# Kernel optimization log

Measured on AMD Instinct MI355X. Metric: run time of the kernel, lower is better.

## Reference

```python
import jax, jax.numpy as jnp
import numpy as np

N_NODES = 100000

def sage_conv(x, src, dst, Wl, bl, Wr):
    # PyG SAGEConv (mean aggr): out = lin_l(mean_{j in N(i)} x_j) + lin_r(x_i)
    msg = x[src]                                            # [E, d] gather
    agg = jax.ops.segment_sum(msg, dst, num_segments=N_NODES)
    cnt = jax.ops.segment_sum(jnp.ones((src.shape[0],), dtype=x.dtype), dst,
                              num_segments=N_NODES)
    agg = agg / jnp.maximum(cnt, 1.0)[:, None]              # mean over neighbors
    return agg @ Wl.T + bl + x @ Wr.T


def setup_inputs() -> dict:
    key = jax.random.key(0)
    ks = jax.random.split(key, 8)
    E = 1600000
    in_c, hid, out_c = 256, 128, 40
    x = jax.random.normal(ks[0], (N_NODES, in_c), dtype=jnp.float32)
    edge_index = jax.random.randint(ks[1], (2, E), 0, N_NODES, dtype=jnp.int64)
    s = 1.0 / np.sqrt(in_c)
    s2 = 1.0 / np.sqrt(hid)
    Wl1 = jax.random.uniform(ks[2], (hid, in_c), jnp.float32, -s, s)
    bl1 = jnp.zeros((hid,), jnp.float32)
    Wr1 = jax.random.uniform(ks[3], (hid, in_c), jnp.float32, -s, s)
    Wl2 = jax.random.uniform(ks[4], (out_c, hid), jnp.float32, -s2, s2)
    bl2 = jnp.zeros((out_c,), jnp.float32)
    Wr2 = jax.random.uniform(ks[5], (out_c, hid), jnp.float32, -s2, s2)
    return {"x": x, "edge_index": edge_index, "Wl1": Wl1, "bl1": bl1,
            "Wr1": Wr1, "Wl2": Wl2, "bl2": bl2, "Wr2": Wr2}


def reference(x, edge_index, Wl1, bl1, Wr1, Wl2, bl2, Wr2):
    src, dst = edge_index[0], edge_index[1]
    h = sage_conv(x, src, dst, Wl1, bl1, Wr1)
    h = jax.nn.relu(h)  # dropout is identity in eval mode
    h = sage_conv(h, src, dst, Wl2, bl2, Wr2)
    return jax.nn.log_softmax(h, axis=-1)
```

## Files before the change

kernel.cpp:

```cpp
#include <hip/hip_runtime.h>
#include <hip/hip_bf16.h>

#define N_NODES 100000
#define IN_C 256
#define HID 128
#define OUT_C 40

#define NPB 9
#define NPP (1 << NPB)
#define NPART ((N_NODES + NPP - 1) >> NPB)
#define CAP 16384

typedef short bf16x8 __attribute__((ext_vector_type(8)));
typedef float f32x4 __attribute__((ext_vector_type(4)));
typedef float f32x2 __attribute__((ext_vector_type(2)));

static __device__ __forceinline__ float bf2f(unsigned short u) {
    return __uint_as_float(((unsigned)u) << 16);
}
static __device__ __forceinline__ unsigned short f2bf(float f) {
    unsigned u = __float_as_uint(f);
    u += 0x7fffu + ((u >> 16) & 1u);
    return (unsigned short)(u >> 16);
}

__global__ __launch_bounds__(256) void cvtw_k(
    const float* __restrict__ Wl1, const float* __restrict__ Wr1,
    const float* __restrict__ Wl2, const float* __restrict__ Wr2,
    unsigned short* __restrict__ W1f, unsigned short* __restrict__ W2f)
{
    int gid = blockIdx.x * 256 + threadIdx.x;
    if (gid < 8192) {
        int g = gid;
        int ln = g & 63, blk = g >> 6;
        int c16 = blk >> 3, ks = blk & 7;
        int col = c16 * 16 + (ln & 15);
        int k0 = ks * 32 + (ln >> 4) * 8;
        const float* src = (col < 128) ? &Wl1[(size_t)col * 256 + k0]
                                       : &Wr1[(size_t)(col - 128) * 256 + k0];
        float4 v0 = *(const float4*)src;
        float4 v1 = *(const float4*)(src + 4);
        bf16x8 a;
        a[0] = (short)f2bf(v0.x); a[1] = (short)f2bf(v0.y);
        a[2] = (short)f2bf(v0.z); a[3] = (short)f2bf(v0.w);
        a[4] = (short)f2bf(v1.x); a[5] = (short)f2bf(v1.y);
        a[6] = (short)f2bf(v1.z); a[7] = (short)f2bf(v1.w);
        *(bf16x8*)&W1f[(size_t)g * 8] = a;
    } else if (gid < 9472) {
        int g = gid - 8192;
        int ln = g & 63, blk = g >> 6;
        int c16 = blk >> 2, ks = blk & 3;
        int col = c16 * 16 + (ln & 15);
        int k0 = ks * 32 + (ln >> 4) * 8;
        const float* src = (col < 40) ? &Wl2[(size_t)col * 128 + k0]
                                      : &Wr2[(size_t)(col - 40) * 128 + k0];
        float4 v0 = *(const float4*)src;
        float4 v1 = *(const float4*)(src + 4);
        bf16x8 a;
        a[0] = (short)f2bf(v0.x); a[1] = (short)f2bf(v0.y);
        a[2] = (short)f2bf(v0.z); a[3] = (short)f2bf(v0.w);
        a[4] = (short)f2bf(v1.x); a[5] = (short)f2bf(v1.y);
        a[6] = (short)f2bf(v1.z); a[7] = (short)f2bf(v1.w);
        *(bf16x8*)&W2f[(size_t)g * 8] = a;
    }
}

__global__ __launch_bounds__(256) void mega1_k(
    const int* __restrict__ ei, int E, int nblkS,
    int* __restrict__ pcnt, unsigned* __restrict__ pairs,
    const float* __restrict__ X,
    const unsigned short* __restrict__ Wf,
    const float* __restrict__ bias,
    unsigned* __restrict__ Yq,
    unsigned short* __restrict__ Zb,
    int M)
{
    constexpr int KP = 264;
    __shared__ unsigned short As[32][KP];
    const int bid = blockIdx.x;
    const int tx = threadIdx.x;

    if (bid < nblkS) {
        int* lh = (int*)&As[0][0];
        int* lb = lh + NPART;
        if (tx < NPART) lh[tx] = 0;
        __syncthreads();
        int base = bid * 4096;
        int n = min(4096, E - base);
        for (int i = tx; i < n; i += 256)
            atomicAdd(&lh[((unsigned)ei[E + base + i]) >> NPB], 1);
        __syncthreads();
        if (tx < NPART) {
            int c = lh[tx];
            lb[tx] = c ? atomicAdd(&pcnt[tx], c) : 0;
            lh[tx] = 0;
        }
        __syncthreads();
        for (int i = tx; i < n; i += 256) {
            unsigned src = (unsigned)ei[base + i];
            unsigned dst = (unsigned)ei[E + base + i];
            int p = dst >> NPB;
            int r = atomicAdd(&lh[p], 1);
            pairs[(size_t)p * CAP + lb[p] + r] = (src << NPB) | (dst & (NPP - 1));
        }
        return;
    }

    const int rowTile = (bid - nblkS) * 32;
    const int wc = tx >> 6, ln = tx & 63;
    const int lc = ln & 15, lk = (ln >> 4) * 8;

    float4 va[4], vb[4];
    #pragma unroll
    for (int i = 0; i < 4; ++i) {
        int g = i * 256 + tx;
        int r = g >> 5, kk = (g & 31) * 8;
        int gr = rowTile + r;
        if (gr < M) {
            const float* p = &X[(size_t)gr * 256 + kk];
            va[i] = *(const float4*)p;
            vb[i] = *(const float4*)(p + 4);
        } else {
            va[i] = make_float4(0.f, 0.f, 0.f, 0.f);
            vb[i] = make_float4(0.f, 0.f, 0.f, 0.f);
        }
    }
    #pragma unroll
    for (int i = 0; i < 4; ++i) {
        int g = i * 256 + tx;
        int r = g >> 5, kk = (g & 31) * 8;
        bf16x8 a;
        a[0] = (short)f2bf(va[i].x); a[1] = (short)f2bf(va[i].y);
        a[2] = (short)f2bf(va[i].z); a[3] = (short)f2bf(va[i].w);
        a[4] = (short)f2bf(vb[i].x); a[5] = (short)f2bf(vb[i].y);
        a[6] = (short)f2bf(vb[i].z); a[7] = (short)f2bf(vb[i].w);
        *(bf16x8*)&As[r][kk] = a;
    }
    __syncthreads();

    f32x4 acc[2][4] = {};
    #pragma unroll
    for (int ks = 0; ks < 8; ++ks) {
        int koff = ks * 32 + lk;
        bf16x8 bfr[4], af[2];
        #pragma unroll
        for (int n = 0; n < 4; ++n)
            bfr[n] = *(const bf16x8*)&Wf[(size_t)(((wc * 4 + n) * 8 + ks) * 512 + ln * 8)];
        #pragma unroll
        for (int m = 0; m < 2; ++m)
            af[m] = *(const bf16x8*)&As[m * 16 + lc][koff];
        #pragma unroll
        for (int m = 0; m < 2; ++m)
            #pragma unroll
            for (int n = 0; n < 4; ++n)
                acc[m][n] = __builtin_amdgcn_mfma_f32_16x16x32_bf16(af[m], bfr[n], acc[m][n], 0, 0, 0);
    }

    __syncthreads();
    const int lr4 = (ln >> 4) * 4;
    #pragma unroll
    for (int m = 0; m < 2; ++m) {
        int r0 = m * 16 + lr4;
        #pragma unroll
        for (int n = 0; n < 4; ++n) {
            int col = wc * 64 + n * 16 + lc;
            float b = (col >= 128) ? bias[col - 128] : 0.f;
            #pragma unroll
            for (int j = 0; j < 4; ++j)
                As[r0 + j][col] = f2bf(acc[m][n][j] + b);
        }
    }
    __syncthreads();
    #pragma unroll
    for (int i = 0; i < 4; ++i) {
        int g = i * 256 + tx;
        int r = g >> 5, c8 = (g & 31) * 8;
        int gr = rowTile + r;
        if (gr >= M) continue;
        bf16x8 v = *(const bf16x8*)&As[r][c8];
        if (c8 < 128) {
            float f0 = bf2f((unsigned short)v[0]), f1 = bf2f((unsigned short)v[1]);
            float f2 = bf2f((unsigned short)v[2]), f3 = bf2f((unsigned short)v[3]);
            float f4 = bf2f((unsigned short)v[4]), f5 = bf2f((unsigned short)v[5]);
            float f6 = bf2f((unsigned short)v[6]), f7 = bf2f((unsigned short)v[7]);
            unsigned lo = __builtin_amdgcn_cvt_pk_fp8_f32(f0, f1, 0, false);
            lo = __builtin_amdgcn_cvt_pk_fp8_f32(f2, f3, lo, true);
            unsigned hi = __builtin_amdgcn_cvt_pk_fp8_f32(f4, f5, 0, false);
            hi = __builtin_amdgcn_cvt_pk_fp8_f32(f6, f7, hi, true);
            uint2 o; o.x = lo; o.y = hi;
            *(uint2*)&Yq[(size_t)gr * 32 + (c8 >> 2)] = o;
        } else {
            *(bf16x8*)&Zb[(size_t)gr * 128 + (c8 - 128)] = v;
        }
    }
}

__global__ __launch_bounds__(256) void pbuild_k(const unsigned* __restrict__ pairs, const int* __restrict__ pcnt,
                                                unsigned* __restrict__ row_info, float* __restrict__ inv,
                                                int* __restrict__ csr, int N) {
    __shared__ int cnt[NPP];
    __shared__ int cur[NPP];
    __shared__ int wsum[4];
    int p = blockIdx.x;
    int ec = pcnt[p];
    size_t base = (size_t)p * CAP;
    int node0 = p << NPB;
    int tid = threadIdx.x;
    cnt[2 * tid] = 0; cnt[2 * tid + 1] = 0;
    __syncthreads();
    for (int e = tid; e < ec; e += 256)
        atomicAdd(&cnt[pairs[base + e] & (NPP - 1)], 1);
    __syncthreads();
    int c0 = cnt[2 * tid], c1 = cnt[2 * tid + 1];
    int s = c0 + c1;
    int lane = tid & 63, w = tid >> 6;
    int ps = s;
    #pragma unroll
    for (int off = 1; off < 64; off <<= 1) { int x = __shfl_up(ps, off); if (lane >= off) ps += x; }
    if (lane == 63) wsum[w] = ps;
    __syncthreads();
    int woff = 0;
    for (int i = 0; i < w; ++i) woff += wsum[i];
    int excl = woff + ps - s;
    int node = node0 + 2 * tid;
    int abeg = (int)base + excl;
    if (node < N) {
        row_info[node] = ((unsigned)abeg << 10) | (unsigned)min(c0, 1023);
        inv[node] = 1.f / fmaxf((float)c0, 1.f);
    }
    if (node + 1 < N) {
        row_info[node + 1] = ((unsigned)(abeg + c0) << 10) | (unsigned)min(c1, 1023);
        inv[node + 1] = 1.f / fmaxf((float)c1, 1.f);
    }
    cur[2 * tid] = excl; cur[2 * tid + 1] = excl + c0;
    __syncthreads();
    for (int e = tid; e < ec; e += 256) {
        unsigned pr = pairs[base + e];
        int r = atomicAdd(&cur[pr & (NPP - 1)], 1);
        csr[base + r] = (int)(pr >> NPB);
    }
}

__global__ __launch_bounds__(256) void gather1_k(const unsigned* __restrict__ row_info, const int* __restrict__ csr,
                                                 const unsigned* __restrict__ Yq,
                                                 unsigned short* __restrict__ Zb,
                                                 const float* __restrict__ inv, int n) {
    int node = blockIdx.x * 16 + (threadIdx.x >> 4);
    if (node >= n) return;
    int t = threadIdx.x & 15;
    unsigned info = row_info[node];
    int beg = (int)(info >> 10), end = beg + (int)(info & 1023);
    float a0 = 0.f, a1 = 0.f, a2 = 0.f, a3 = 0.f;
    float a4 = 0.f, a5 = 0.f, a6 = 0.f, a7 = 0.f;
    int e = beg;
    for (; e + 2 <= end; e += 2) {
        int s0 = csr[e], s1 = csr[e + 1];
        uint2 u0 = *(const uint2*)&Yq[(size_t)s0 * 32 + t * 2];
        uint2 u1 = *(const uint2*)&Yq[(size_t)s1 * 32 + t * 2];
        f32x2 p;
        p = __builtin_amdgcn_cvt_pk_f32_fp8(u0.x, false); a0 += p[0]; a1 += p[1];
        p = __builtin_amdgcn_cvt_pk_f32_fp8(u0.x, true);  a2 += p[0]; a3 += p[1];
        p = __builtin_amdgcn_cvt_pk_f32_fp8(u0.y, false); a4 += p[0]; a5 += p[1];
        p = __builtin_amdgcn_cvt_pk_f32_fp8(u0.y, true);  a6 += p[0]; a7 += p[1];
        p = __builtin_amdgcn_cvt_pk_f32_fp8(u1.x, false); a0 += p[0]; a1 += p[1];
        p = __builtin_amdgcn_cvt_pk_f32_fp8(u1.x, true);  a2 += p[0]; a3 += p[1];
        p = __builtin_amdgcn_cvt_pk_f32_fp8(u1.y, false); a4 += p[0]; a5 += p[1];
        p = __builtin_amdgcn_cvt_pk_f32_fp8(u1.y, true);  a6 += p[0]; a7 += p[1];
    }
    if (e < end) {
        uint2 u0 = *(const uint2*)&Yq[(size_t)csr[e] * 32 + t * 2];
        f32x2 p;
        p = __builtin_amdgcn_cvt_pk_f32_fp8(u0.x, false); a0 += p[0]; a1 += p[1];
        p = __builtin_amdgcn_cvt_pk_f32_fp8(u0.x, true);  a2 += p[0]; a3 += p[1];
        p = __builtin_amdgcn_cvt_pk_f32_fp8(u0.y, false); a4 += p[0]; a5 += p[1];
        p = __builtin_amdgcn_cvt_pk_f32_fp8(u0.y, true);  a6 += p[0]; a7 += p[1];
    }
    float iv = inv[node];
    bf16x8 z = *(const bf16x8*)&Zb[(size_t)node * HID + t * 8];
    bf16x8 h;
    h[0] = (short)f2bf(fmaxf(a0 * iv + bf2f((unsigned short)z[0]), 0.f));
    h[1] = (short)f2bf(fmaxf(a1 * iv + bf2f((unsigned short)z[1]), 0.f));
    h[2] = (short)f2bf(fmaxf(a2 * iv + bf2f((unsigned short)z[2]), 0.f));
    h[3] = (short)f2bf(fmaxf(a3 * iv + bf2f((unsigned short)z[3]), 0.f));
    h[4] = (short)f2bf(fmaxf(a4 * iv + bf2f((unsigned short)z[4]), 0.f));
    h[5] = (short)f2bf(fmaxf(a5 * iv + bf2f((unsigned short)z[5]), 0.f));
    h[6] = (short)f2bf(fmaxf(a6 * iv + bf2f((unsigned short)z[6]), 0.f));
    h[7] = (short)f2bf(fmaxf(a7 * iv + bf2f((unsigned short)z[7]), 0.f));
    *(bf16x8*)&Zb[(size_t)node * HID + t * 8] = h;
}

__global__ __launch_bounds__(256) void gemm2_k(
    const unsigned short* __restrict__ Hb,
    const unsigned short* __restrict__ Wf,
    const float* __restrict__ bias,
    unsigned* __restrict__ Y2q,
    unsigned short* __restrict__ Z2b,
    int M)
{
    constexpr int KP = 136;
    __shared__ unsigned short As[128][KP];
    const int tx = threadIdx.x;
    const int rowTile = blockIdx.x * 128;
    const int wv = tx >> 6, ln = tx & 63;
    const int lc = ln & 15, lk = (ln >> 4) * 8;

    #pragma unroll
    for (int i = 0; i < 8; ++i) {
        int g = i * 256 + tx;
        int r = g >> 4, kk = (g & 15) * 8;
        int gr = rowTile + r;
        bf16x8 a = {};
        if (gr < M) a = *(const bf16x8*)&Hb[(size_t)gr * 128 + kk];
        *(bf16x8*)&As[r][kk] = a;
    }
    __syncthreads();

    f32x4 acc[2][5] = {};
    #pragma unroll
    for (int ks = 0; ks < 4; ++ks) {
        int koff = ks * 32 + lk;
        bf16x8 bfr[5], af[2];
        #pragma unroll
        for (int n = 0; n < 5; ++n)
            bfr[n] = *(const bf16x8*)&Wf[(size_t)((n * 4 + ks) * 512 + ln * 8)];
        #pragma unroll
        for (int m = 0; m < 2; ++m)
            af[m] = *(const bf16x8*)&As[wv * 32 + m * 16 + lc][koff];
        #pragma unroll
        for (int m = 0; m < 2; ++m)
            #pragma unroll
            for (int n = 0; n < 5; ++n)
                acc[m][n] = __builtin_amdgcn_mfma_f32_16x16x32_bf16(af[m], bfr[n], acc[m][n], 0, 0, 0);
    }

    __syncthreads();
    unsigned short (*OutL)[96] = (unsigned short (*)[96])&As[0][0];
    const int lr4 = (ln >> 4) * 4;
    #pragma unroll
    for (int m = 0; m < 2; ++m) {
        int r0 = wv * 32 + m * 16 + lr4;
        #pragma unroll
        for (int n = 0; n < 5; ++n) {
            int col = n * 16 + lc;
            float b = (col >= 40) ? bias[col - 40] : 0.f;
            #pragma unroll
            for (int j = 0; j < 4; ++j)
                OutL[r0 + j][col] = f2bf(acc[m][n][j] + b);
        }
    }
    __syncthreads();
    #pragma unroll
    for (int i = 0; i < 5; ++i) {
        int g = i * 256 + tx;
        int r = g / 10, cg = g % 10;
        int c8 = cg * 8;
        int gr = rowTile + r;
        if (gr >= M) continue;
        bf16x8 v = *(const bf16x8*)&OutL[r][c8];
        if (c8 < 40) {
            float f0 = bf2f((unsigned short)v[0]), f1 = bf2f((unsigned short)v[1]);
            float f2 = bf2f((unsigned short)v[2]), f3 = bf2f((unsigned short)v[3]);
            float f4 = bf2f((unsigned short)v[4]), f5 = bf2f((unsigned short)v[5]);
            float f6 = bf2f((unsigned short)v[6]), f7 = bf2f((unsigned short)v[7]);
            unsigned lo = __builtin_amdgcn_cvt_pk_fp8_f32(f0, f1, 0, false);
            lo = __builtin_amdgcn_cvt_pk_fp8_f32(f2, f3, lo, true);
            unsigned hi = __builtin_amdgcn_cvt_pk_fp8_f32(f4, f5, 0, false);
            hi = __builtin_amdgcn_cvt_pk_fp8_f32(f6, f7, hi, true);
            uint2 o; o.x = lo; o.y = hi;
            *(uint2*)&Y2q[(size_t)gr * 10 + (c8 >> 2)] = o;
        } else {
            *(bf16x8*)&Z2b[(size_t)gr * 40 + (c8 - 40)] = v;
        }
    }
}

__global__ __launch_bounds__(256) void gather2_logsm_k(const unsigned* __restrict__ row_info, const int* __restrict__ csr,
                                                       const unsigned* __restrict__ Y2q,
                                                       const unsigned short* __restrict__ Zb,
                                                       const float* __restrict__ inv,
                                                       float* __restrict__ out, int n) {
    int node = blockIdx.x * 16 + (threadIdx.x >> 4);
    if (node >= n) return;
    int t = threadIdx.x & 15;
    float4 v = make_float4(-INFINITY, -INFINITY, -INFINITY, -INFINITY);
    if (t < 10) {
        unsigned info = row_info[node];
        int beg = (int)(info >> 10), end = beg + (int)(info & 1023);
        float a0 = 0.f, a1 = 0.f, a2 = 0.f, a3 = 0.f;
        for (int e = beg; e < end; ++e) {
            unsigned u = Y2q[(size_t)csr[e] * 10 + t];
            f32x2 p;
            p = __builtin_amdgcn_cvt_pk_f32_fp8(u, false); a0 += p[0]; a1 += p[1];
            p = __builtin_amdgcn_cvt_pk_f32_fp8(u, true);  a2 += p[0]; a3 += p[1];
        }
        float iv = inv[node];
        ushort4 z = *(const ushort4*)&Zb[(size_t)node * OUT_C + t * 4];
        v.x = a0 * iv + bf2f(z.x); v.y = a1 * iv + bf2f(z.y);
        v.z = a2 * iv + bf2f(z.z); v.w = a3 * iv + bf2f(z.w);
    }
    float m = fmaxf(fmaxf(v.x, v.y), fmaxf(v.z, v.w));
    #pragma unroll
    for (int off = 8; off; off >>= 1) m = fmaxf(m, __shfl_xor(m, off, 16));
    float s4 = 0.f;
    if (t < 10) s4 = expf(v.x - m) + expf(v.y - m) + expf(v.z - m) + expf(v.w - m);
    #pragma unroll
    for (int off = 8; off; off >>= 1) s4 += __shfl_xor(s4, off, 16);
    float ls = m + logf(s4);
    if (t < 10) {
        float4 o;
        o.x = v.x - ls; o.y = v.y - ls; o.z = v.z - ls; o.w = v.w - ls;
        *(float4*)&out[(size_t)node * OUT_C + t * 4] = o;
    }
}

extern "C" void kernel_launch(void* const* d_in, const int* in_sizes, int n_in,
                              void* d_out, int out_size, void* d_ws, size_t ws_size,
                              hipStream_t stream) {
    const float* x   = (const float*)d_in[0];
    const int*   ei  = (const int*)d_in[1];
    const float* Wl1 = (const float*)d_in[2];
    const float* bl1 = (const float*)d_in[3];
    const float* Wr1 = (const float*)d_in[4];
    const float* Wl2 = (const float*)d_in[5];
    const float* bl2 = (const float*)d_in[6];
    const float* Wr2 = (const float*)d_in[7];
    float* out = (float*)d_out;
    const int N = N_NODES;
    const int E = in_sizes[1] / 2;

    char* ws = (char*)d_ws;
    int*      pcnt     = (int*)(ws + 0x0000);
    unsigned* row_info = (unsigned*)(ws + 0x10000);
    float*    inv      = (float*)(ws + 0x80000);
    int*      csr      = (int*)(ws + 0x100000);
    unsigned* pairs    = (unsigned*)(ws + 0xE00000);
    unsigned short* Z2b = (unsigned short*)(ws + 0xE00000);
    unsigned short* W1f = (unsigned short*)(ws + 0x1B00000);
    unsigned short* W2f = (unsigned short*)(ws + 0x1B60000);
    unsigned* Yq1   = (unsigned*)(ws + 0x1C00000);
    unsigned short* Z1b = (unsigned short*)(ws + 0x3500000);
    unsigned* Y2q   = (unsigned*)(ws + 0x5200000);

    hipMemsetAsync(pcnt, 0, NPART * 4, stream);

    cvtw_k<<<37, 256, 0, stream>>>(Wl1, Wr1, Wl2, Wr2, W1f, W2f);

    int nblkS = (E + 4095) / 4096;
    int nblkG = (N + 31) / 32;
    mega1_k<<<nblkS + nblkG, 256, 0, stream>>>(ei, E, nblkS, pcnt, pairs,
                                               x, W1f, bl1, Yq1, Z1b, N);

    pbuild_k<<<NPART, 256, 0, stream>>>(pairs, pcnt, row_info, inv, csr, N);

    gather1_k<<<(N + 15) / 16, 256, 0, stream>>>(row_info, csr, Yq1, Z1b, inv, N);

    gemm2_k<<<(N + 127) / 128, 256, 0, stream>>>(Z1b, W2f, bl2, Y2q, Z2b, N);

    gather2_logsm_k<<<(N + 15) / 16, 256, 0, stream>>>(row_info, csr, Y2q, Z2b, inv, out, N);
}
```

Before: 184.9 us.

## Reorder mega1 block roles, raise MFMA priority, widen pbuild to 512 threads

Three separate tweaks. The fused mega1 kernel now runs its GEMM row-tile blocks first and the edge-scatter blocks after them, which changes how work is scheduled across CUs. s_setprio brackets the MFMA loops in both GEMM kernels so those waves get issue priority. pbuild uses 512 threads with one node per thread instead of 256 threads handling two nodes each, which shortens the serial per-thread work and widens the scan and atomic loops, at some cost in occupancy and launch shape.

```diff
diff --git a/kernel.cpp b/kernel.cpp
--- a/kernel.cpp
+++ b/kernel.cpp
@@ -66,7 +66,7 @@
 }
 
 __global__ __launch_bounds__(256) void mega1_k(
-    const int* __restrict__ ei, int E, int nblkS,
+    const int* __restrict__ ei, int E, int nblkG,
     int* __restrict__ pcnt, unsigned* __restrict__ pairs,
     const float* __restrict__ X,
     const unsigned short* __restrict__ Wf,
@@ -80,12 +80,12 @@
     const int bid = blockIdx.x;
     const int tx = threadIdx.x;
 
-    if (bid < nblkS) {
+    if (bid >= nblkG) {
         int* lh = (int*)&As[0][0];
         int* lb = lh + NPART;
         if (tx < NPART) lh[tx] = 0;
         __syncthreads();
-        int base = bid * 4096;
+        int base = (bid - nblkG) * 4096;
         int n = min(4096, E - base);
         for (int i = tx; i < n; i += 256)
             atomicAdd(&lh[((unsigned)ei[E + base + i]) >> NPB], 1);
@@ -106,7 +106,7 @@
         return;
     }
 
-    const int rowTile = (bid - nblkS) * 32;
+    const int rowTile = bid * 32;
     const int wc = tx >> 6, ln = tx & 63;
     const int lc = ln & 15, lk = (ln >> 4) * 8;
 
@@ -149,11 +149,13 @@
         #pragma unroll
         for (int m = 0; m < 2; ++m)
             af[m] = *(const bf16x8*)&As[m * 16 + lc][koff];
+        __builtin_amdgcn_s_setprio(1);
         #pragma unroll
         for (int m = 0; m < 2; ++m)
             #pragma unroll
             for (int n = 0; n < 4; ++n)
                 acc[m][n] = __builtin_amdgcn_mfma_f32_16x16x32_bf16(af[m], bfr[n], acc[m][n], 0, 0, 0);
+        __builtin_amdgcn_s_setprio(0);
     }
 
     __syncthreads();
@@ -195,46 +197,41 @@
     }
 }
 
-__global__ __launch_bounds__(256) void pbuild_k(const unsigned* __restrict__ pairs, const int* __restrict__ pcnt,
+__global__ __launch_bounds__(512) void pbuild_k(const unsigned* __restrict__ pairs, const int* __restrict__ pcnt,
                                                 unsigned* __restrict__ row_info, float* __restrict__ inv,
                                                 int* __restrict__ csr, int N) {
     __shared__ int cnt[NPP];
     __shared__ int cur[NPP];
-    __shared__ int wsum[4];
+    __shared__ int wsum[8];
     int p = blockIdx.x;
     int ec = pcnt[p];
     size_t base = (size_t)p * CAP;
     int node0 = p << NPB;
     int tid = threadIdx.x;
-    cnt[2 * tid] = 0; cnt[2 * tid + 1] = 0;
-    __syncthreads();
-    for (int e = tid; e < ec; e += 256)
+    cnt[tid] = 0;
+    __syncthreads();
+    for (int e = tid; e < ec; e += 512)
         atomicAdd(&cnt[pairs[base + e] & (NPP - 1)], 1);
     __syncthreads();
-    int c0 = cnt[2 * tid], c1 = cnt[2 * tid + 1];
-    int s = c0 + c1;
+    int c0 = cnt[tid];
     int lane = tid & 63, w = tid >> 6;
-    int ps = s;
+    int ps = c0;
     #pragma unroll
     for (int off = 1; off < 64; off <<= 1) { int x = __shfl_up(ps, off); if (lane >= off) ps += x; }
     if (lane == 63) wsum[w] = ps;
     __syncthreads();
     int woff = 0;
     for (int i = 0; i < w; ++i) woff += wsum[i];
-    int excl = woff + ps - s;
-    int node = node0 + 2 * tid;
+    int excl = woff + ps - c0;
+    int node = node0 + tid;
     int abeg = (int)base + excl;
     if (node < N) {
         row_info[node] = ((unsigned)abeg << 10) | (unsigned)min(c0, 1023);
         inv[node] = 1.f / fmaxf((float)c0, 1.f);
     }
-    if (node + 1 < N) {
-        row_info[node + 1] = ((unsigned)(abeg + c0) << 10) | (unsigned)min(c1, 1023);
-        inv[node + 1] = 1.f / fmaxf((float)c1, 1.f);
-    }
-    cur[2 * tid] = excl; cur[2 * tid + 1] = excl + c0;
-    __syncthreads();
-    for (int e = tid; e < ec; e += 256) {
+    cur[tid] = excl;
+    __syncthreads();
+    for (int e = tid; e < ec; e += 512) {
         unsigned pr = pairs[base + e];
         int r = atomicAdd(&cur[pr & (NPP - 1)], 1);
         csr[base + r] = (int)(pr >> NPB);
@@ -326,11 +323,13 @@
         #pragma unroll
         for (int m = 0; m < 2; ++m)
             af[m] = *(const bf16x8*)&As[wv * 32 + m * 16 + lc][koff];
+        __builtin_amdgcn_s_setprio(1);
         #pragma unroll
         for (int m = 0; m < 2; ++m)
             #pragma unroll
             for (int n = 0; n < 5; ++n)
                 acc[m][n] = __builtin_amdgcn_mfma_f32_16x16x32_bf16(af[m], bfr[n], acc[m][n], 0, 0, 0);
+        __builtin_amdgcn_s_setprio(0);
     }
 
     __syncthreads();
@@ -447,10 +446,10 @@
 
     int nblkS = (E + 4095) / 4096;
     int nblkG = (N + 31) / 32;
-    mega1_k<<<nblkS + nblkG, 256, 0, stream>>>(ei, E, nblkS, pcnt, pairs,
+    mega1_k<<<nblkG + nblkS, 256, 0, stream>>>(ei, E, nblkG, pcnt, pairs,
                                                x, W1f, bl1, Yq1, Z1b, N);
 
-    pbuild_k<<<NPART, 256, 0, stream>>>(pairs, pcnt, row_info, inv, csr, N);
+    pbuild_k<<<NPART, 512, 0, stream>>>(pairs, pcnt, row_info, inv, csr, N);
 
     gather1_k<<<(N + 15) / 16, 256, 0, stream>>>(row_info, csr, Yq1, Z1b, inv, N);
 
```

Result: no change. 185.6 us (+0.4%).
